# Kernel optimization log

Hardware: AMD Instinct MI355X
Metric: run time of the kernel (lower is better)

## Reference

```python
import jax, jax.numpy as jnp
import numpy as np

B, N, E, H = 8, 512, 256, 8
DK = E // H
DIST_BAR = (0.3, 0.7, 1e10)  # init dist_bar + [1e10] appended in forward
NEG = -1e10


def setup_inputs() -> dict:
    key = jax.random.key(0)
    ks = jax.random.split(key, 24)
    s = 0.02
    inp = {
        'query': jax.random.normal(ks[0], (B, N, E), jnp.float32),
        'key':   jax.random.normal(ks[1], (B, N, E), jnp.float32),
        'value': jax.random.normal(ks[2], (B, N, E), jnp.float32),
        'dist':  jax.random.uniform(ks[3], (B, N, N), jnp.float32),
        'mask':  jax.random.randint(ks[4], (B, N, N), 0, 2).astype(jnp.int32),
        # 4 linears (q, k, v, out), stored as [in, out] for x @ W
        'Wq': jax.random.normal(ks[5], (E, E)) * s, 'bq': jnp.zeros((E,)),
        'Wk': jax.random.normal(ks[6], (E, E)) * s, 'bk': jnp.zeros((E,)),
        'Wv': jax.random.normal(ks[7], (E, E)) * s, 'bv': jnp.zeros((E,)),
        'Wo': jax.random.normal(ks[8], (E, E)) * s, 'bo': jnp.zeros((E,)),
        # cnn: Conv2d(1,H,1) -> ReLU -> Conv2d(H,H,1); 1x1 convs = per-pixel linear maps
        'cw1': jax.random.normal(ks[9], (H,)) * s,     'cb1': jnp.zeros((H,)),
        'cw2': jax.random.normal(ks[10], (H, H)) * s,  'cb2': jnp.zeros((H,)),
        # scale_linear: Linear(3E, E) -> ReLU -> Linear(E, E)
        'Ws1': jax.random.normal(ks[11], (3 * E, E)) * s, 'bs1': jnp.zeros((E,)),
        'Ws2': jax.random.normal(ks[12], (E, E)) * s,     'bs2': jnp.zeros((E,)),
    }
    return inp


def reference(query, key, value, dist, mask,
              Wq, bq, Wk, bk, Wv, bv, Wo, bo,
              cw1, cb1, cw2, cb2, Ws1, bs1, Ws2, bs2):
    def heads(x, W, b):  # [B,N,E] -> [B,H,N,DK]
        return (x @ W + b).reshape(B, N, H, DK).transpose(0, 2, 1, 3)

    q, k, v = heads(query, Wq, bq), heads(key, Wk, bk), heads(value, Wv, bv)
    d4 = dist[:, None]  # [B,1,N,N]
    # 1x1 conv stack: [B,1,N,N] -> [B,H,N,N]
    c1 = jax.nn.relu(d4 * cw1[None, :, None, None] + cb1[None, :, None, None])
    dist_conv = jnp.einsum('oi,bijk->bojk', cw2, c1) + cb2[None, :, None, None]

    scores = jnp.einsum('bhqd,bhkd->bhqk', q, k) / np.sqrt(DK).astype(np.float32)
    scores = scores * dist_conv
    scores = jnp.where(mask[:, None] == 0, NEG, scores)

    outs = []
    for bar in DIST_BAR:
        dm = d4 < bar                       # [B,1,N,N] bool
        dm = dm.at[:, :, 0, :].set(True).at[:, :, :, 0].set(True)
        s = jnp.where(dm, scores, NEG)
        p = jax.nn.softmax(s, axis=-1)      # [B,H,N,N]
        o = jnp.einsum('bhqk,bhkd->bhqd', p, v)
        o = o.transpose(0, 2, 1, 3).reshape(B, N, E)
        outs.append(o @ Wo + bo)
    x = jnp.concatenate(outs, axis=-1)      # [B,N,3E]
    h1 = jax.nn.relu(x @ Ws1 + bs1)
    return h1 @ Ws2 + bs2                   # [B,N,E]
```

## Files before the change

### kernel.cpp

```cpp
#include <hip/hip_runtime.h>
#include <math.h>

typedef _Float16 h16;
typedef __attribute__((ext_vector_type(8))) _Float16 h16x8;
typedef __attribute__((ext_vector_type(4))) float f32x4;
typedef unsigned long long u64t;
typedef unsigned int u32t;
typedef unsigned char u8t;

__global__ __launch_bounds__(256) void prep_k(
    const float* __restrict__ Wq, const float* __restrict__ Wk,
    const float* __restrict__ Wv, const float* __restrict__ Ws2,
    const float* __restrict__ Ws1, const float* __restrict__ bo,
    const float* __restrict__ bs1, h16* __restrict__ WT,
    float* __restrict__ bcomb)
{
    const int bid = blockIdx.x;
    __shared__ float T[32][33];
    if (bid < 448) {
        const int z = bid >> 6, idx = bid & 63;
        const float* in = (z == 0) ? Wq : (z == 1) ? Wk : (z == 2) ? Wv :
                          (z == 3) ? Ws2 : (Ws1 + (size_t)(z - 4) * 65536);
        h16* out = WT + (size_t)z * 65536;
        const int t = threadIdx.x, tx = t & 31, ty = t >> 5;
        const int r0 = (idx >> 3) * 32, c0 = (idx & 7) * 32;
        #pragma unroll
        for (int i = 0; i < 4; ++i)
            T[ty + i * 8][tx] = in[(size_t)(r0 + ty + i * 8) * 256 + c0 + tx];
        __syncthreads();
        #pragma unroll
        for (int i = 0; i < 4; ++i)
            out[(size_t)(c0 + ty + i * 8) * 256 + r0 + tx] = (h16)T[tx][ty + i * 8];
    } else {
        const int j = threadIdx.x;
        float acc = bs1[j];
        for (int r = 0; r < 768; ++r)
            acc = fmaf(bo[r & 255], Ws1[(size_t)r * 256 + j], acc);
        bcomb[j] = acc;
    }
}

__global__ __launch_bounds__(256) void qkvw_k(
    const float* __restrict__ Xq, const float* __restrict__ Xk,
    const float* __restrict__ Xv, const float* __restrict__ Wo,
    const h16* __restrict__ WT,
    const float* __restrict__ bq, const float* __restrict__ bk,
    const float* __restrict__ bv,
    h16* __restrict__ qb, h16* __restrict__ kb, h16* __restrict__ vbT,
    h16* __restrict__ WbigT)
{
    const int bid = blockIdx.x;
    const float* A; const h16* Bt; const float* bias = nullptr;
    int mode, row0, col0, sgm = 0;
    if (bid < 768) {
        const int z = bid >> 8, r = bid & 255;
        row0 = (r & 63) * 64; col0 = (r >> 6) * 64;
        A = (z == 0) ? Xq : (z == 1) ? Xk : Xv;
        Bt = WT + (size_t)z * 65536;
        bias = (z == 0) ? bq : (z == 1) ? bk : bv;
        mode = z;
    } else {
        const int r = bid - 768;
        sgm = r >> 4; const int tt = r & 15;
        row0 = (tt >> 2) * 64; col0 = (tt & 3) * 64;
        A = Wo; Bt = WT + (size_t)(4 + sgm) * 65536; mode = 3;
    }

    __shared__ __align__(16) h16 As[2][64][40];
    __shared__ __align__(16) h16 Bs[2][64][40];
    const int t = threadIdx.x, w = t >> 6, lane = t & 63;
    const int Q = lane >> 4, n = lane & 15;
    const int sr = t >> 2, sc = (t & 3) * 8;

    auto ldA = [&](int k0) -> h16x8 {
        const float* ap = A + (size_t)(row0 + sr) * 256 + k0 + sc;
        float4 f0 = *(const float4*)ap;
        float4 f1 = *(const float4*)(ap + 4);
        h16x8 hv;
        hv[0] = (h16)f0.x; hv[1] = (h16)f0.y; hv[2] = (h16)f0.z; hv[3] = (h16)f0.w;
        hv[4] = (h16)f1.x; hv[5] = (h16)f1.y; hv[6] = (h16)f1.z; hv[7] = (h16)f1.w;
        return hv;
    };
    auto ldB = [&](int k0) -> h16x8 {
        return *(const h16x8*)(Bt + (size_t)(col0 + sr) * 256 + k0 + sc);
    };

    {
        h16x8 a0 = ldA(0), b0 = ldB(0);
        *(h16x8*)&As[0][sr][sc] = a0;
        *(h16x8*)&Bs[0][sr][sc] = b0;
    }
    __syncthreads();

    f32x4 acc4[4];
    #pragma unroll
    for (int c = 0; c < 4; ++c) acc4[c] = (f32x4){0.f, 0.f, 0.f, 0.f};

    for (int it = 0; it < 8; ++it) {
        const int cur = it & 1;
        h16x8 arN, brN;
        if (it < 7) { arN = ldA(32 * (it + 1)); brN = ldB(32 * (it + 1)); }
        h16x8 af = *(const h16x8*)&As[cur][w * 16 + n][Q * 8];
        #pragma unroll
        for (int cg = 0; cg < 4; ++cg) {
            h16x8 bf = *(const h16x8*)&Bs[cur][cg * 16 + n][Q * 8];
            acc4[cg] = __builtin_amdgcn_mfma_f32_16x16x32_f16(af, bf, acc4[cg], 0, 0, 0);
        }
        if (it < 7) {
            *(h16x8*)&As[cur ^ 1][sr][sc] = arN;
            *(h16x8*)&Bs[cur ^ 1][sr][sc] = brN;
        }
        __syncthreads();
    }

    if (mode < 2) {
        h16* out = mode ? kb : qb;
        #pragma unroll
        for (int cg = 0; cg < 4; ++cg) {
            const float bvv = bias[col0 + cg * 16 + n];
            #pragma unroll
            for (int r = 0; r < 4; ++r)
                out[(size_t)(row0 + w * 16 + 4 * Q + r) * 256 + col0 + cg * 16 + n] =
                    (h16)(acc4[cg][r] + bvv);
        }
    } else if (mode == 2) {
        const int bb = row0 >> 9;
        #pragma unroll
        for (int cg = 0; cg < 4; ++cg) {
            const float bvv = bias[col0 + cg * 16 + n];
            const int col = col0 + cg * 16 + n;
            #pragma unroll
            for (int r = 0; r < 4; ++r) {
                const int m = row0 + w * 16 + 4 * Q + r;
                vbT[((size_t)(bb * 256 + col)) * 512 + (m & 511)] = (h16)(acc4[cg][r] + bvv);
            }
        }
    } else {
        #pragma unroll
        for (int cg = 0; cg < 4; ++cg) {
            const int col = col0 + cg * 16 + n;
            #pragma unroll
            for (int r = 0; r < 4; ++r)
                WbigT[(size_t)col * 768 + sgm * 256 + row0 + w * 16 + 4 * Q + r] =
                    (h16)acc4[cg][r];
        }
    }
}

template<int OUT16RELU>
__global__ __launch_bounds__(256) void hgemm32_k(
    const h16* __restrict__ A, const h16* __restrict__ Bt,
    const float* __restrict__ bias, void* __restrict__ outv, int K)
{
    __shared__ __align__(16) h16 As[2][32][72];
    __shared__ __align__(16) h16 Bs[2][64][72];
    const int t = threadIdx.x, w = t >> 6, lane = t & 63;
    const int Q = lane >> 4, n = lane & 15;
    const int row0 = blockIdx.x * 32, col0 = blockIdx.y * 64;
    const int r16 = (w & 1) * 16, c32 = (w >> 1) * 32;
    const int asr = t >> 3, asc = (t & 7) * 8;
    const int bsr = t >> 2, bsc = (t & 3) * 16;

    auto ldA = [&](int k0) -> h16x8 {
        return *(const h16x8*)(A + (size_t)(row0 + asr) * K + k0 + asc);
    };
    auto ldB0 = [&](int k0) -> h16x8 {
        return *(const h16x8*)(Bt + (size_t)(col0 + bsr) * K + k0 + bsc);
    };
    auto ldB1 = [&](int k0) -> h16x8 {
        return *(const h16x8*)(Bt + (size_t)(col0 + bsr) * K + k0 + bsc + 8);
    };

    {
        h16x8 a0 = ldA(0), b0 = ldB0(0), b1 = ldB1(0);
        *(h16x8*)&As[0][asr][asc] = a0;
        *(h16x8*)&Bs[0][bsr][bsc] = b0;
        *(h16x8*)&Bs[0][bsr][bsc + 8] = b1;
    }
    __syncthreads();

    f32x4 acc2[2];
    acc2[0] = (f32x4){0.f, 0.f, 0.f, 0.f};
    acc2[1] = (f32x4){0.f, 0.f, 0.f, 0.f};
    const int iters = K >> 6;

    for (int it = 0; it < iters; ++it) {
        const int cur = it & 1;
        h16x8 arN, brN0, brN1;
        if (it + 1 < iters) {
            arN = ldA(64 * (it + 1));
            brN0 = ldB0(64 * (it + 1));
            brN1 = ldB1(64 * (it + 1));
        }
        #pragma unroll
        for (int kh = 0; kh < 2; ++kh) {
            h16x8 af = *(const h16x8*)&As[cur][r16 + n][kh * 32 + Q * 8];
            #pragma unroll
            for (int cg = 0; cg < 2; ++cg) {
                h16x8 bf = *(const h16x8*)&Bs[cur][c32 + cg * 16 + n][kh * 32 + Q * 8];
                acc2[cg] = __builtin_amdgcn_mfma_f32_16x16x32_f16(af, bf, acc2[cg], 0, 0, 0);
            }
        }
        if (it + 1 < iters) {
            *(h16x8*)&As[cur ^ 1][asr][asc] = arN;
            *(h16x8*)&Bs[cur ^ 1][bsr][bsc] = brN0;
            *(h16x8*)&Bs[cur ^ 1][bsr][bsc + 8] = brN1;
        }
        __syncthreads();
    }

    #pragma unroll
    for (int cg = 0; cg < 2; ++cg) {
        const int col = col0 + c32 + cg * 16 + n;
        const float bv = bias[col];
        #pragma unroll
        for (int r = 0; r < 4; ++r) {
            const int row = row0 + r16 + 4 * Q + r;
            if (OUT16RELU)
                ((h16*)outv)[(size_t)row * 256 + col] = (h16)fmaxf(acc2[cg][r] + bv, 0.f);
            else
                ((float*)outv)[(size_t)row * 256 + col] = acc2[cg][r] + bv;
        }
    }
}

__global__ __launch_bounds__(256, 2) void attn_k(
    const h16* __restrict__ qb, const h16* __restrict__ kb,
    const h16* __restrict__ vbT,
    const float* __restrict__ dist, const int* __restrict__ mask,
    const float* __restrict__ cw1, const float* __restrict__ cb1,
    const float* __restrict__ cw2, const float* __restrict__ cb2,
    h16* __restrict__ OB)
{
    const int bx = blockIdx.x, b = bx >> 5, q0 = (bx & 31) * 16;
    const int hg = blockIdx.y;
    const int t = threadIdx.x, w = t >> 6, lane = t & 63;
    const int Q = lane >> 4, n = lane & 15;
    const int h = hg * 4 + w;

    __shared__ __align__(16) h16 Ft[2][4][16][68];
    __shared__ __align__(16) u8t Cd[2][16][72];
    __shared__ __align__(16) h16 Sx[4][16][72];

    const float invs = 0.17677669529663687f;
    float w1[8], b1[8];
    #pragma unroll
    for (int u = 0; u < 8; ++u) { w1[u] = cw1[u]; b1[u] = cb1[u]; }
    float w2a[4][8], fba[4];
    #pragma unroll
    for (int hh = 0; hh < 4; ++hh) {
        #pragma unroll
        for (int u = 0; u < 8; ++u) w2a[hh][u] = invs * cw2[(hg * 4 + hh) * 8 + u];
        fba[hh] = invs * cb2[hg * 4 + hh];
    }

    const h16x8 aq =
        *(const h16x8*)(qb + ((size_t)(b * 512 + q0 + n)) * 256 + h * 32 + Q * 8);

    const f32x4 z4 = {0.f, 0.f, 0.f, 0.f};
    f32x4 acc[3][2];
    #pragma unroll
    for (int s = 0; s < 3; ++s) { acc[s][0] = z4; acc[s][1] = z4; }
    float mprev = -3e38f;
    float lsum[3] = {0.f, 0.f, 0.f};

    const int scol = lane;

    auto stage = [&](int buf, int kkb, const float* dp, const int* mp) {
        #pragma unroll
        for (int i = 0; i < 4; ++i) {
            const int row = w + 4 * i;
            const float d = dp[i];
            const bool fr = ((q0 + row) == 0) || ((kkb + scol) == 0);
            const bool keep = (mp[i] != 0);
            const u32t code = (keep && (fr || d < 0.3f) ? 1u : 0u)
                            | (keep && (fr || d < 0.7f) ? 2u : 0u)
                            | (keep ? 4u : 0u);
            Cd[buf][row][scol] = (u8t)code;
            float ch[8];
            #pragma unroll
            for (int u = 0; u < 8; ++u) ch[u] = fmaxf(fmaf(d, w1[u], b1[u]), 0.f);
            #pragma unroll
            for (int hh = 0; hh < 4; ++hh) {
                float f = fba[hh];
                #pragma unroll
                for (int u = 0; u < 8; ++u) f = fmaf(ch[u], w2a[hh][u], f);
                Ft[buf][hh][row][scol] = (h16)f;
            }
        }
    };

    float dv[4]; int mkv[4];
    #pragma unroll
    for (int i = 0; i < 4; ++i) {
        const size_t off = ((size_t)(b * 512 + q0 + w + 4 * i)) * 512 + scol;
        dv[i] = dist[off]; mkv[i] = mask[off];
    }
    h16x8 kf[4], vf[4];
    #pragma unroll
    for (int cg = 0; cg < 4; ++cg)
        kf[cg] = *(const h16x8*)(kb + ((size_t)(b * 512 + cg * 16 + n)) * 256 + h * 32 + Q * 8);
    #pragma unroll
    for (int nh = 0; nh < 2; ++nh)
        #pragma unroll
        for (int k2 = 0; k2 < 2; ++k2)
            vf[nh * 2 + k2] = *(const h16x8*)(
                vbT + ((size_t)((b * 8 + h) * 32 + nh * 16 + n)) * 512 + k2 * 32 + Q * 8);
    stage(0, 0, dv, mkv);
    __syncthreads();

    for (int kc = 0; kc < 8; ++kc) {
        const int cur = kc & 1, kk0 = kc * 64;

        float dN[4]; int mkN[4]; h16x8 kfN[4], vfN[4];
        if (kc < 7) {
            const int kn = kk0 + 64;
            #pragma unroll
            for (int i = 0; i < 4; ++i) {
                const size_t off = ((size_t)(b * 512 + q0 + w + 4 * i)) * 512 + kn + scol;
                dN[i] = dist[off]; mkN[i] = mask[off];
            }
            #pragma unroll
            for (int cg = 0; cg < 4; ++cg)
                kfN[cg] = *(const h16x8*)(
                    kb + ((size_t)(b * 512 + kn + cg * 16 + n)) * 256 + h * 32 + Q * 8);
            #pragma unroll
            for (int nh = 0; nh < 2; ++nh)
                #pragma unroll
                for (int k2 = 0; k2 < 2; ++k2)
                    vfN[nh * 2 + k2] = *(const h16x8*)(
                        vbT + ((size_t)((b * 8 + h) * 32 + nh * 16 + n)) * 512
                            + kn + k2 * 32 + Q * 8);
        }

        f32x4 s4[4];
        #pragma unroll
        for (int cg = 0; cg < 4; ++cg)
            s4[cg] = __builtin_amdgcn_mfma_f32_16x16x32_f16(aq, kf[cg], z4, 0, 0, 0);

        #pragma unroll
        for (int cg = 0; cg < 4; ++cg)
            #pragma unroll
            for (int r = 0; r < 4; ++r) {
                const float f = (float)Ft[cur][w][4 * Q + r][cg * 16 + n];
                Sx[w][4 * Q + r][cg * 16 + n] = (h16)(s4[cg][r] * f);
            }
        __builtin_amdgcn_wave_barrier();

        const u64t cd0 = *(const u64t*)&Cd[cur][n][Q * 8];
        const u64t cd1 = *(const u64t*)&Cd[cur][n][32 + Q * 8];
        float sv[16];
        {
            h16x8 s0 = *(const h16x8*)&Sx[w][n][Q * 8];
            h16x8 s1 = *(const h16x8*)&Sx[w][n][32 + Q * 8];
            #pragma unroll
            for (int j = 0; j < 8; ++j) { sv[j] = (float)s0[j]; sv[8 + j] = (float)s1[j]; }
        }
        float cm = -3e38f;
        #pragma unroll
        for (int i = 0; i < 16; ++i) {
            const u32t cc = (u32t)((i < 8 ? cd0 : cd1) >> (8 * (i & 7))) & 7u;
            cm = fmaxf(cm, (cc & 4u) ? sv[i] : -3e38f);
        }
        cm = fmaxf(cm, __shfl_xor(cm, 16));
        cm = fmaxf(cm, __shfl_xor(cm, 32));
        const float mnew = fmaxf(mprev, cm);
        const float alphaA = __expf(mprev - mnew);
        mprev = mnew;

        #pragma unroll
        for (int r = 0; r < 4; ++r) {
            const float aR = __shfl(alphaA, 4 * Q + r);
            #pragma unroll
            for (int s = 0; s < 3; ++s) { acc[s][0][r] *= aR; acc[s][1][r] *= aR; }
        }

        h16x8 pf[3][2];
        float l0 = 0.f, l1 = 0.f, l2 = 0.f;
        #pragma unroll
        for (int i = 0; i < 16; ++i) {
            const u32t cc = (u32t)((i < 8 ? cd0 : cd1) >> (8 * (i & 7))) & 7u;
            const float e = __expf(sv[i] - mnew);
            const float p0 = (cc & 1u) ? e : 0.f;
            const float p1 = (cc & 2u) ? e : 0.f;
            const float p2 = (cc & 4u) ? e : 0.f;
            l0 += p0; l1 += p1; l2 += p2;
            pf[0][i >> 3][i & 7] = (h16)p0;
            pf[1][i >> 3][i & 7] = (h16)p1;
            pf[2][i >> 3][i & 7] = (h16)p2;
        }
        lsum[0] = lsum[0] * alphaA + l0;
        lsum[1] = lsum[1] * alphaA + l1;
        lsum[2] = lsum[2] * alphaA + l2;

        #pragma unroll
        for (int k2 = 0; k2 < 2; ++k2)
            #pragma unroll
            for (int nh = 0; nh < 2; ++nh)
                #pragma unroll
                for (int s = 0; s < 3; ++s)
                    acc[s][nh] = __builtin_amdgcn_mfma_f32_16x16x32_f16(
                        pf[s][k2], vf[nh * 2 + k2], acc[s][nh], 0, 0, 0);

        if (kc < 7) {
            stage(cur ^ 1, kk0 + 64, dN, mkN);
            #pragma unroll
            for (int i = 0; i < 4; ++i) { kf[i] = kfN[i]; vf[i] = vfN[i]; dv[i] = dN[i]; mkv[i] = mkN[i]; }
        }
        __syncthreads();
    }

    float lrow[3];
    #pragma unroll
    for (int s = 0; s < 3; ++s) {
        float lv = lsum[s];
        lv += __shfl_xor(lv, 16);
        lv += __shfl_xor(lv, 32);
        lrow[s] = lv;
    }
    #pragma unroll
    for (int s = 0; s < 3; ++s) {
        #pragma unroll
        for (int r = 0; r < 4; ++r) {
            const float il = 1.0f / __shfl(lrow[s], 4 * Q + r);
            const size_t row = (size_t)(b * 512 + q0 + 4 * Q + r);
            h16* op = OB + row * 768 + s * 256 + h * 32 + n;
            op[0]  = (h16)(acc[s][0][r] * il);
            op[16] = (h16)(acc[s][1][r] * il);
        }
    }
}

extern "C" void kernel_launch(void* const* d_in, const int* in_sizes, int n_in,
                              void* d_out, int out_size, void* d_ws, size_t ws_size,
                              hipStream_t stream)
{
    const float* query = (const float*)d_in[0];
    const float* key   = (const float*)d_in[1];
    const float* value = (const float*)d_in[2];
    const float* dist  = (const float*)d_in[3];
    const int*   mask  = (const int*)d_in[4];
    const float* Wq = (const float*)d_in[5];  const float* bq = (const float*)d_in[6];
    const float* Wk = (const float*)d_in[7];  const float* bk = (const float*)d_in[8];
    const float* Wv = (const float*)d_in[9];  const float* bv = (const float*)d_in[10];
    const float* Wo = (const float*)d_in[11]; const float* bo = (const float*)d_in[12];
    const float* cw1 = (const float*)d_in[13]; const float* cb1 = (const float*)d_in[14];
    const float* cw2 = (const float*)d_in[15]; const float* cb2 = (const float*)d_in[16];
    const float* Ws1 = (const float*)d_in[17]; const float* bs1 = (const float*)d_in[18];
    const float* Ws2 = (const float*)d_in[19]; const float* bs2 = (const float*)d_in[20];

    h16* qb    = (h16*)d_ws;
    h16* kb    = qb + 1048576;
    h16* vbT   = kb + 1048576;
    h16* OB    = vbT + 1048576;
    h16* h1    = OB + 3145728;
    h16* WT    = h1 + 1048576;
    h16* WbigT = WT + 458752;
    float* bcomb = (float*)(WbigT + 196608);

    prep_k<<<dim3(449), 256, 0, stream>>>(Wq, Wk, Wv, Ws2, Ws1, bo, bs1, WT, bcomb);

    qkvw_k<<<dim3(816), 256, 0, stream>>>(query, key, value, Wo, WT,
                                          bq, bk, bv, qb, kb, vbT, WbigT);

    attn_k<<<dim3(256, 2), 256, 0, stream>>>(qb, kb, vbT, dist, mask,
                                             cw1, cb1, cw2, cb2, OB);

    hgemm32_k<1><<<dim3(128, 4), 256, 0, stream>>>(OB, WbigT, bcomb, h1, 768);
    hgemm32_k<0><<<dim3(128, 4), 256, 0, stream>>>(h1, WT + 3 * 65536, bs2, d_out, 256);
}
```

Measured before the change: 182.9 us.

## Replace per-element conv stack with piecewise-linear LUT and split bias reduction

The 1x1 conv stack (ReLU of 8 affine maps, then an 8x8 mix) is a piecewise-linear function of dist. prep_k now precomputes the ReLU breakpoints and a slope/intercept table per head and segment. attn_k counts breakpoints and does one FMA per head instead of about 40 FMAs, and Ft is relaid out so the four head values are written with one vector store. The serial 768-step bias fold in prep_k is also split across 16 blocks, with the partial sums added in the hgemm epilogue. This adds a shared-memory table lookup and a small amount of extra bias summation.

```diff
diff --git a/kernel.cpp b/kernel.cpp
--- a/kernel.cpp
+++ b/kernel.cpp
@@ -2,6 +2,7 @@
 #include <math.h>
 
 typedef _Float16 h16;
+typedef __attribute__((ext_vector_type(4))) _Float16 h16x4;
 typedef __attribute__((ext_vector_type(8))) _Float16 h16x8;
 typedef __attribute__((ext_vector_type(4))) float f32x4;
 typedef unsigned long long u64t;
@@ -12,8 +13,11 @@
     const float* __restrict__ Wq, const float* __restrict__ Wk,
     const float* __restrict__ Wv, const float* __restrict__ Ws2,
     const float* __restrict__ Ws1, const float* __restrict__ bo,
-    const float* __restrict__ bs1, h16* __restrict__ WT,
-    float* __restrict__ bcomb)
+    const float* __restrict__ bs1,
+    const float* __restrict__ cw1, const float* __restrict__ cb1,
+    const float* __restrict__ cw2, const float* __restrict__ cb2,
+    h16* __restrict__ WT, float* __restrict__ bcombP,
+    float* __restrict__ tthr, float* __restrict__ fLUT)
 {
     const int bid = blockIdx.x;
     __shared__ float T[32][33];
@@ -31,12 +35,54 @@
         #pragma unroll
         for (int i = 0; i < 4; ++i)
             out[(size_t)(c0 + ty + i * 8) * 256 + r0 + tx] = (h16)T[tx][ty + i * 8];
+    } else if (bid < 464) {
+        const int z = bid - 448;
+        const int j = threadIdx.x;
+        float acc = (z == 0) ? bs1[j] : 0.f;
+        const int r0 = z * 48;
+        #pragma unroll 4
+        for (int r = r0; r < r0 + 48; ++r)
+            acc = fmaf(bo[r & 255], Ws1[(size_t)r * 256 + j], acc);
+        bcombP[z * 256 + j] = acc;
     } else {
-        const int j = threadIdx.x;
-        float acc = bs1[j];
-        for (int r = 0; r < 768; ++r)
-            acc = fmaf(bo[r & 255], Ws1[(size_t)r * 256 + j], acc);
-        bcomb[j] = acc;
+        const int t = threadIdx.x;
+        const float INVS = 0.17677669529663687f;
+        float tv[8]; int zu[8];
+        #pragma unroll
+        for (int u = 0; u < 8; ++u) {
+            const float w = cw1[u];
+            zu[u] = (w == 0.f) ? 1 : 0;
+            tv[u] = zu[u] ? 3.0e38f : (-cb1[u] / w);
+        }
+        if (t < 8) tthr[t] = tv[t];
+        if (t < 72) {
+            const int h = t & 7, jj = t >> 3;
+            int rank[8];
+            #pragma unroll
+            for (int u = 0; u < 8; ++u) {
+                int rk = 0;
+                #pragma unroll
+                for (int v = 0; v < 8; ++v)
+                    rk += ((tv[v] < tv[u]) || (tv[v] == tv[u] && v < u)) ? 1 : 0;
+                rank[u] = rk;
+            }
+            float slope = 0.f, inter = cb2[h];
+            #pragma unroll
+            for (int u = 0; u < 8; ++u) {
+                const float c2 = cw2[h * 8 + u];
+                if (zu[u]) {
+                    inter += c2 * fmaxf(cb1[u], 0.f);
+                } else {
+                    const bool act = (cw1[u] > 0.f) ? (rank[u] < jj) : (rank[u] >= jj);
+                    if (act) {
+                        slope = fmaf(c2, cw1[u], slope);
+                        inter = fmaf(c2, cb1[u], inter);
+                    }
+                }
+            }
+            float2 e; e.x = INVS * slope; e.y = INVS * inter;
+            ((float2*)fLUT)[jj * 8 + h] = e;
+        }
     }
 }
 
@@ -150,7 +196,7 @@
 template<int OUT16RELU>
 __global__ __launch_bounds__(256) void hgemm32_k(
     const h16* __restrict__ A, const h16* __restrict__ Bt,
-    const float* __restrict__ bias, void* __restrict__ outv, int K)
+    const float* __restrict__ bias, void* __restrict__ outv, int K, int nbp)
 {
     __shared__ __align__(16) h16 As[2][32][72];
     __shared__ __align__(16) h16 Bs[2][64][72];
@@ -212,7 +258,8 @@
     #pragma unroll
     for (int cg = 0; cg < 2; ++cg) {
         const int col = col0 + c32 + cg * 16 + n;
-        const float bv = bias[col];
+        float bv = bias[col];
+        for (int p = 1; p < nbp; ++p) bv += bias[p * 256 + col];
         #pragma unroll
         for (int r = 0; r < 4; ++r) {
             const int row = row0 + r16 + 4 * Q + r;
@@ -228,8 +275,7 @@
     const h16* __restrict__ qb, const h16* __restrict__ kb,
     const h16* __restrict__ vbT,
     const float* __restrict__ dist, const int* __restrict__ mask,
-    const float* __restrict__ cw1, const float* __restrict__ cb1,
-    const float* __restrict__ cw2, const float* __restrict__ cb2,
+    const float* __restrict__ tthr, const float* __restrict__ fLUT,
     h16* __restrict__ OB)
 {
     const int bx = blockIdx.x, b = bx >> 5, q0 = (bx & 31) * 16;
@@ -238,21 +284,19 @@
     const int Q = lane >> 4, n = lane & 15;
     const int h = hg * 4 + w;
 
-    __shared__ __align__(16) h16 Ft[2][4][16][68];
+    __shared__ __align__(16) h16 Ft[2][16][66][4];
     __shared__ __align__(16) u8t Cd[2][16][72];
     __shared__ __align__(16) h16 Sx[4][16][72];
-
-    const float invs = 0.17677669529663687f;
-    float w1[8], b1[8];
-    #pragma unroll
-    for (int u = 0; u < 8; ++u) { w1[u] = cw1[u]; b1[u] = cb1[u]; }
-    float w2a[4][8], fba[4];
-    #pragma unroll
-    for (int hh = 0; hh < 4; ++hh) {
-        #pragma unroll
-        for (int u = 0; u < 8; ++u) w2a[hh][u] = invs * cw2[(hg * 4 + hh) * 8 + u];
-        fba[hh] = invs * cb2[hg * 4 + hh];
-    }
+    __shared__ __align__(8)  float2 lutS[4][9];
+
+    float th[8];
+    #pragma unroll
+    for (int u = 0; u < 8; ++u) th[u] = tthr[u];
+    if (t < 36) {
+        const int hh = t / 9, j = t - hh * 9;
+        lutS[hh][j] = ((const float2*)fLUT)[j * 8 + hg * 4 + hh];
+    }
+    __syncthreads();
 
     const h16x8 aq =
         *(const h16x8*)(qb + ((size_t)(b * 512 + q0 + n)) * 256 + h * 32 + Q * 8);
@@ -271,22 +315,22 @@
         for (int i = 0; i < 4; ++i) {
             const int row = w + 4 * i;
             const float d = dp[i];
+            int idx = 0;
+            #pragma unroll
+            for (int u = 0; u < 8; ++u) idx += (d > th[u]) ? 1 : 0;
             const bool fr = ((q0 + row) == 0) || ((kkb + scol) == 0);
             const bool keep = (mp[i] != 0);
             const u32t code = (keep && (fr || d < 0.3f) ? 1u : 0u)
                             | (keep && (fr || d < 0.7f) ? 2u : 0u)
                             | (keep ? 4u : 0u);
             Cd[buf][row][scol] = (u8t)code;
-            float ch[8];
-            #pragma unroll
-            for (int u = 0; u < 8; ++u) ch[u] = fmaxf(fmaf(d, w1[u], b1[u]), 0.f);
+            h16x4 fv;
             #pragma unroll
             for (int hh = 0; hh < 4; ++hh) {
-                float f = fba[hh];
-                #pragma unroll
-                for (int u = 0; u < 8; ++u) f = fmaf(ch[u], w2a[hh][u], f);
-                Ft[buf][hh][row][scol] = (h16)f;
-            }
+                const float2 si = lutS[hh][idx];
+                fv[hh] = (h16)fmaf(d, si.x, si.y);
+            }
+            *(h16x4*)&Ft[buf][row][scol][0] = fv;
         }
     };
 
@@ -342,7 +386,7 @@
         for (int cg = 0; cg < 4; ++cg)
             #pragma unroll
             for (int r = 0; r < 4; ++r) {
-                const float f = (float)Ft[cur][w][4 * Q + r][cg * 16 + n];
+                const float f = (float)Ft[cur][4 * Q + r][cg * 16 + n][w];
                 Sx[w][4 * Q + r][cg * 16 + n] = (h16)(s4[cg][r] * f);
             }
         __builtin_amdgcn_wave_barrier();
@@ -456,16 +500,19 @@
     h16* h1    = OB + 3145728;
     h16* WT    = h1 + 1048576;
     h16* WbigT = WT + 458752;
-    float* bcomb = (float*)(WbigT + 196608);
-
-    prep_k<<<dim3(449), 256, 0, stream>>>(Wq, Wk, Wv, Ws2, Ws1, bo, bs1, WT, bcomb);
+    float* bcombP = (float*)(WbigT + 196608);
+    float* tthr   = bcombP + 4096;
+    float* fLUT   = tthr + 8;
+
+    prep_k<<<dim3(465), 256, 0, stream>>>(Wq, Wk, Wv, Ws2, Ws1, bo, bs1,
+                                          cw1, cb1, cw2, cb2, WT, bcombP, tthr, fLUT);
 
     qkvw_k<<<dim3(816), 256, 0, stream>>>(query, key, value, Wo, WT,
                                           bq, bk, bv, qb, kb, vbT, WbigT);
 
     attn_k<<<dim3(256, 2), 256, 0, stream>>>(qb, kb, vbT, dist, mask,
-                                             cw1, cb1, cw2, cb2, OB);
-
-    hgemm32_k<1><<<dim3(128, 4), 256, 0, stream>>>(OB, WbigT, bcomb, h1, 768);
-    hgemm32_k<0><<<dim3(128, 4), 256, 0, stream>>>(h1, WT + 3 * 65536, bs2, d_out, 256);
+                                             tthr, fLUT, OB);
+
+    hgemm32_k<1><<<dim3(128, 4), 256, 0, stream>>>(OB, WbigT, bcombP, h1, 768, 16);
+    hgemm32_k<0><<<dim3(128, 4), 256, 0, stream>>>(h1, WT + 3 * 65536, bs2, d_out, 256, 1);
 }
```

New measurement: 166.0 us. -9.2%, faster.
